# Performance work log

Hardware: AMD Instinct MI355X
Metric: run time of the kernel (lower is better)

The kernel has to match this reference:

```python
import jax, jax.numpy as jnp
import numpy as np

STRIDE = (2, 2)
PADDING = (1, 1)
OUTPUT_PADDING = (0, 0)


def setup_inputs() -> dict:
    key = jax.random.key(0)
    k1, k2, k3 = jax.random.split(key, 3)
    B, Cin, H, W = 16, 32, 128, 128
    Cout, Kh, Kw = 32, 4, 4
    signal = jax.random.normal(k1, (B, Cin, H, W), dtype=jnp.float32)
    # conv_transpose weight layout: (Cin, Cout/groups, Kh, Kw)
    weight = jax.random.normal(k2, (Cin, Cout, Kh, Kw), dtype=jnp.float32) * 0.05
    bias = jax.random.normal(k3, (Cout,), dtype=jnp.float32)
    return {"signal": signal, "weight": weight, "bias": bias}


def reference(signal, weight, bias):
    """FFT-based 2D transposed convolution (stride 2, padding 1, groups=1, dilation=1).

    Matches torch.nn.functional.conv_transpose2d semantics:
      y[n] = sum_m x[m] * w[n - m*s], cropped by `padding` on each side.
    """
    sh, sw = STRIDE
    ph, pw = PADDING
    oph, opw = OUTPUT_PADDING
    B, Cin, H, W = signal.shape
    _, Cout, Kh, Kw = weight.shape

    # 1) zero-stuff the input by the stride (lhs dilation)
    Hu, Wu = (H - 1) * sh + 1, (W - 1) * sw + 1
    xu = jnp.zeros((B, Cin, Hu, Wu), dtype=signal.dtype)
    xu = xu.at[:, :, ::sh, ::sw].set(signal)

    # 2) full (true) convolution of upsampled signal with the weight via rFFT
    Nh, Nw = Hu + Kh - 1, Wu + Kw - 1  # full-conv output size == FFT size
    Xf = jnp.fft.rfft2(xu, s=(Nh, Nw))          # (B, Cin, Nh, Nw//2+1) complex64
    Wf = jnp.fft.rfft2(weight, s=(Nh, Nw))      # (Cin, Cout, Nh, Nw//2+1) complex64
    Yf = jnp.einsum('bihw,iohw->bohw', Xf, Wf)  # contract over input channels
    y = jnp.fft.irfft2(Yf, s=(Nh, Nw))          # (B, Cout, Nh, Nw) float32

    # 3) crop by padding; output_padding extends the end (zero here)
    out_h = (H - 1) * sh - 2 * ph + Kh + oph
    out_w = (W - 1) * sw - 2 * pw + Kw + opw
    y = y[:, :, ph:ph + out_h, pw:pw + out_w]

    # 4) bias
    return y + bias[None, :, None, None]
```

## Files before the change

kernel.cpp:

```cpp
#include <hip/hip_runtime.h>

#define B_    16
#define CIN   32
#define H_    128
#define W_    128
#define COUT  32
#define OH_   256
#define OW_   256

typedef __attribute__((ext_vector_type(8))) short bf8_t;
typedef __attribute__((ext_vector_type(4))) float f32x4;

__device__ inline unsigned int f2bf(float f) {
    unsigned int u = __float_as_uint(f);
    return (u + 0x7fffu + ((u >> 16) & 1u)) >> 16;
}

__global__ __launch_bounds__(256)
void prep_w(const float* __restrict__ wgt, unsigned short* __restrict__ wt) {
    int e = blockIdx.x * 256 + threadIdx.x;
    int khkw = e >> 10, co = (e >> 5) & 31, ci = e & 31;
    wt[e] = (unsigned short)f2bf(wgt[(ci * COUT + co) * 16 + khkw]);
}

__global__ __launch_bounds__(512, 4)
void convt_fused(const float* __restrict__ x,
                 const unsigned short* __restrict__ wt,
                 const float* __restrict__ bias,
                 float* __restrict__ y) {
    __shared__ unsigned short xs[6 * 66 * 32];

    const int tid  = threadIdx.x;
    const int lane = tid & 63;
    const int wv   = tid >> 6;
    const int n    = blockIdx.z;
    const int t0   = blockIdx.y * 4;
    const int u0   = blockIdx.x * 64;

#pragma unroll
    for (int j = 0; j < 3; ++j) {
        const int c  = wv + j * 8;
        const int hr = c >> 2, gp = c & 3;
        const int ih = t0 - 1 + hr;
        const int iw = u0 - 1 + lane;
        const bool inb = ((unsigned)ih < H_) && ((unsigned)iw < W_);
        const float* xq = x + (((long)(n * CIN + gp * 8) * H_ + ih) * W_ + iw);
        float v[8];
#pragma unroll
        for (int k = 0; k < 8; ++k)
            v[k] = inb ? xq[(long)k * (H_ * W_)] : 0.0f;
        uint4 pk;
        pk.x = f2bf(v[0]) | (f2bf(v[1]) << 16);
        pk.y = f2bf(v[2]) | (f2bf(v[3]) << 16);
        pk.z = f2bf(v[4]) | (f2bf(v[5]) << 16);
        pk.w = f2bf(v[6]) | (f2bf(v[7]) << 16);
        const int slot = gp ^ ((iw >> 1) & 3);
        *(uint4*)(xs + (hr * 66 + lane) * 32 + slot * 8) = pk;
    }
    if (tid < 48) {
        const int c  = tid >> 1;
        const int hr = c >> 2, gp = c & 3;
        const int wc = 64 + (tid & 1);
        const int ih = t0 - 1 + hr;
        const int iw = u0 - 1 + wc;
        const bool inb = ((unsigned)ih < H_) && ((unsigned)iw < W_);
        const float* xq = x + (((long)(n * CIN + gp * 8) * H_ + ih) * W_ + iw);
        float v[8];
#pragma unroll
        for (int k = 0; k < 8; ++k)
            v[k] = inb ? xq[(long)k * (H_ * W_)] : 0.0f;
        uint4 pk;
        pk.x = f2bf(v[0]) | (f2bf(v[1]) << 16);
        pk.y = f2bf(v[2]) | (f2bf(v[3]) << 16);
        pk.z = f2bf(v[4]) | (f2bf(v[5]) << 16);
        pk.w = f2bf(v[6]) | (f2bf(v[7]) << 16);
        const int slot = gp ^ ((iw >> 1) & 3);
        *(uint4*)(xs + (hr * 66 + wc) * 32 + slot * 8) = pk;
    }

    const int ch   = wv & 1;
    const int trow = wv >> 1;
    const int g    = lane >> 4;
    const int li   = lane & 15;

    float bias4[4];
#pragma unroll
    for (int r = 0; r < 4; ++r) bias4[r] = bias[ch * 16 + g * 4 + r];

    __syncthreads();

    const int t = t0 + trow;
    const unsigned short* wp = wt + (ch * 16 + li) * 32 + g * 8;

#pragma unroll
    for (int po = 0; po < 2; ++po) {
        const int kh0 = po ? 0 : 1, dh0 = po ? 2 : 1;
        const int kh1 = po ? 2 : 3, dh1 = po ? 1 : 0;

        bf8_t wfA[4], wfB[4];
#pragma unroll
        for (int kw = 0; kw < 4; ++kw) {
            wfA[kw] = *(const bf8_t*)(wp + (kh0 * 4 + kw) * 1024);
            wfB[kw] = *(const bf8_t*)(wp + (kh1 * 4 + kw) * 1024);
        }

#pragma unroll
        for (int st = 0; st < 4; ++st) {
            const int us = u0 + st * 16;

            bf8_t xfA[3], xfB[3];
#pragma unroll
            for (int dw = 0; dw < 3; ++dw) {
                const int wg   = us + li + dw - 1;
                const int wl   = wg - (u0 - 1);
                const int slot = g ^ ((wg >> 1) & 3);
                xfA[dw] = *(const bf8_t*)(xs + ((trow + dh0) * 66 + wl) * 32 + slot * 8);
                xfB[dw] = *(const bf8_t*)(xs + ((trow + dh1) * 66 + wl) * 32 + slot * 8);
            }

            f32x4 acc[2];
#pragma unroll
            for (int qo = 0; qo < 2; ++qo)
                acc[qo] = (f32x4){bias4[0], bias4[1], bias4[2], bias4[3]};

#pragma unroll
            for (int qo = 0; qo < 2; ++qo) {
                const int dw0 = qo ? 2 : 1, kw0 = qo ? 0 : 1;
                const int dw1 = qo ? 1 : 0, kw1 = qo ? 2 : 3;
                acc[qo] = __builtin_amdgcn_mfma_f32_16x16x32_bf16(
                    wfA[kw0], xfA[dw0], acc[qo], 0, 0, 0);
                acc[qo] = __builtin_amdgcn_mfma_f32_16x16x32_bf16(
                    wfA[kw1], xfA[dw1], acc[qo], 0, 0, 0);
                acc[qo] = __builtin_amdgcn_mfma_f32_16x16x32_bf16(
                    wfB[kw0], xfB[dw0], acc[qo], 0, 0, 0);
                acc[qo] = __builtin_amdgcn_mfma_f32_16x16x32_bf16(
                    wfB[kw1], xfB[dw1], acc[qo], 0, 0, 0);
            }

            const int oh = 2 * t + po;
#pragma unroll
            for (int r = 0; r < 4; ++r) {
                const int co = ch * 16 + g * 4 + r;
                float* yp = y + (((long)(n * COUT + co) * OH_ + oh) * OW_) + 2 * (us + li);
                *(float2*)yp = make_float2(acc[0][r], acc[1][r]);
            }
        }
    }
}

extern "C" void kernel_launch(void* const* d_in, const int* in_sizes, int n_in,
                              void* d_out, int out_size, void* d_ws, size_t ws_size,
                              hipStream_t stream) {
    const float* x = (const float*)d_in[0];
    const float* w = (const float*)d_in[1];
    const float* b = (const float*)d_in[2];
    float* y = (float*)d_out;

    unsigned short* wt = (unsigned short*)d_ws;

    prep_w<<<64, 256, 0, stream>>>(w, wt);
    convt_fused<<<dim3(W_ / 64, H_ / 4, B_), 512, 0, stream>>>(x, wt, b, y);
}
```

Before: 169.2 us.

## Double-buffer input tiles so each block prefetches its second row group during compute

```diff
diff --git a/kernel.cpp b/kernel.cpp
--- a/kernel.cpp
+++ b/kernel.cpp
@@ -23,59 +23,114 @@
     wt[e] = (unsigned short)f2bf(wgt[(ci * COUT + co) * 16 + khkw]);
 }
 
+__device__ __forceinline__ void issue8(const float* __restrict__ x, int n, int tt0,
+                                       int u0, int c, int cell, float v[8]) {
+    const int hr = c >> 2, gp = c & 3;
+    const int ih = tt0 - 1 + hr;
+    const int iw = u0 - 1 + cell;
+    const bool inb = ((unsigned)ih < H_) && ((unsigned)iw < W_);
+    const float* xq = x + (((long)(n * CIN + gp * 8) * H_ + ih) * W_ + iw);
+#pragma unroll
+    for (int k = 0; k < 8; ++k)
+        v[k] = inb ? xq[(long)k * (H_ * W_)] : 0.0f;
+}
+
+__device__ __forceinline__ void pack_write(unsigned short* __restrict__ xsb, int u0,
+                                           int c, int cell, const float v[8]) {
+    const int hr = c >> 2, gp = c & 3;
+    const int iw = u0 - 1 + cell;
+    uint4 pk;
+    pk.x = f2bf(v[0]) | (f2bf(v[1]) << 16);
+    pk.y = f2bf(v[2]) | (f2bf(v[3]) << 16);
+    pk.z = f2bf(v[4]) | (f2bf(v[5]) << 16);
+    pk.w = f2bf(v[6]) | (f2bf(v[7]) << 16);
+    const int slot = gp ^ ((iw >> 1) & 3);
+    *(uint4*)(xsb + (hr * 66 + cell) * 32 + slot * 8) = pk;
+}
+
+__device__ __forceinline__ void compute_po(const unsigned short* __restrict__ xsb,
+                                           const unsigned short* __restrict__ wp,
+                                           const float bias4[4], int n, int tt0,
+                                           int trow, int u0, int ch, int g, int li,
+                                           int po, float* __restrict__ y) {
+    const int kh0 = po ? 0 : 1, dh0 = po ? 2 : 1;
+    const int kh1 = po ? 2 : 3, dh1 = po ? 1 : 0;
+
+    bf8_t wfA[4], wfB[4];
+#pragma unroll
+    for (int kw = 0; kw < 4; ++kw) {
+        wfA[kw] = *(const bf8_t*)(wp + (kh0 * 4 + kw) * 1024);
+        wfB[kw] = *(const bf8_t*)(wp + (kh1 * 4 + kw) * 1024);
+    }
+
+    const int t = tt0 + trow;
+#pragma unroll
+    for (int st = 0; st < 4; ++st) {
+        const int us = u0 + st * 16;
+
+        bf8_t xfA[3], xfB[3];
+#pragma unroll
+        for (int dw = 0; dw < 3; ++dw) {
+            const int wg   = us + li + dw - 1;
+            const int wl   = wg - (u0 - 1);
+            const int slot = g ^ ((wg >> 1) & 3);
+            xfA[dw] = *(const bf8_t*)(xsb + ((trow + dh0) * 66 + wl) * 32 + slot * 8);
+            xfB[dw] = *(const bf8_t*)(xsb + ((trow + dh1) * 66 + wl) * 32 + slot * 8);
+        }
+
+        f32x4 acc[2];
+#pragma unroll
+        for (int qo = 0; qo < 2; ++qo)
+            acc[qo] = (f32x4){bias4[0], bias4[1], bias4[2], bias4[3]};
+
+#pragma unroll
+        for (int qo = 0; qo < 2; ++qo) {
+            const int dw0 = qo ? 2 : 1, kw0 = qo ? 0 : 1;
+            const int dw1 = qo ? 1 : 0, kw1 = qo ? 2 : 3;
+            acc[qo] = __builtin_amdgcn_mfma_f32_16x16x32_bf16(
+                wfA[kw0], xfA[dw0], acc[qo], 0, 0, 0);
+            acc[qo] = __builtin_amdgcn_mfma_f32_16x16x32_bf16(
+                wfA[kw1], xfA[dw1], acc[qo], 0, 0, 0);
+            acc[qo] = __builtin_amdgcn_mfma_f32_16x16x32_bf16(
+                wfB[kw0], xfB[dw0], acc[qo], 0, 0, 0);
+            acc[qo] = __builtin_amdgcn_mfma_f32_16x16x32_bf16(
+                wfB[kw1], xfB[dw1], acc[qo], 0, 0, 0);
+        }
+
+        const int oh = 2 * t + po;
+#pragma unroll
+        for (int r = 0; r < 4; ++r) {
+            const int co = ch * 16 + g * 4 + r;
+            float* yp = y + (((long)(n * COUT + co) * OH_ + oh) * OW_) + 2 * (us + li);
+            *(float2*)yp = make_float2(acc[0][r], acc[1][r]);
+        }
+    }
+}
+
 __global__ __launch_bounds__(512, 4)
 void convt_fused(const float* __restrict__ x,
                  const unsigned short* __restrict__ wt,
                  const float* __restrict__ bias,
                  float* __restrict__ y) {
-    __shared__ unsigned short xs[6 * 66 * 32];
+    __shared__ unsigned short xs[2][6 * 66 * 32];
 
     const int tid  = threadIdx.x;
     const int lane = tid & 63;
     const int wv   = tid >> 6;
     const int n    = blockIdx.z;
-    const int t0   = blockIdx.y * 4;
+    const int tb   = blockIdx.y * 8;
     const int u0   = blockIdx.x * 64;
 
 #pragma unroll
     for (int j = 0; j < 3; ++j) {
-        const int c  = wv + j * 8;
-        const int hr = c >> 2, gp = c & 3;
-        const int ih = t0 - 1 + hr;
-        const int iw = u0 - 1 + lane;
-        const bool inb = ((unsigned)ih < H_) && ((unsigned)iw < W_);
-        const float* xq = x + (((long)(n * CIN + gp * 8) * H_ + ih) * W_ + iw);
         float v[8];
-#pragma unroll
-        for (int k = 0; k < 8; ++k)
-            v[k] = inb ? xq[(long)k * (H_ * W_)] : 0.0f;
-        uint4 pk;
-        pk.x = f2bf(v[0]) | (f2bf(v[1]) << 16);
-        pk.y = f2bf(v[2]) | (f2bf(v[3]) << 16);
-        pk.z = f2bf(v[4]) | (f2bf(v[5]) << 16);
-        pk.w = f2bf(v[6]) | (f2bf(v[7]) << 16);
-        const int slot = gp ^ ((iw >> 1) & 3);
-        *(uint4*)(xs + (hr * 66 + lane) * 32 + slot * 8) = pk;
+        issue8(x, n, tb, u0, wv + j * 8, lane, v);
+        pack_write(xs[0], u0, wv + j * 8, lane, v);
     }
     if (tid < 48) {
-        const int c  = tid >> 1;
-        const int hr = c >> 2, gp = c & 3;
-        const int wc = 64 + (tid & 1);
-        const int ih = t0 - 1 + hr;
-        const int iw = u0 - 1 + wc;
-        const bool inb = ((unsigned)ih < H_) && ((unsigned)iw < W_);
-        const float* xq = x + (((long)(n * CIN + gp * 8) * H_ + ih) * W_ + iw);
         float v[8];
-#pragma unroll
-        for (int k = 0; k < 8; ++k)
-            v[k] = inb ? xq[(long)k * (H_ * W_)] : 0.0f;
-        uint4 pk;
-        pk.x = f2bf(v[0]) | (f2bf(v[1]) << 16);
-        pk.y = f2bf(v[2]) | (f2bf(v[3]) << 16);
-        pk.z = f2bf(v[4]) | (f2bf(v[5]) << 16);
-        pk.w = f2bf(v[6]) | (f2bf(v[7]) << 16);
-        const int slot = gp ^ ((iw >> 1) & 3);
-        *(uint4*)(xs + (hr * 66 + wc) * 32 + slot * 8) = pk;
+        issue8(x, n, tb, u0, tid >> 1, 64 + (tid & 1), v);
+        pack_write(xs[0], u0, tid >> 1, 64 + (tid & 1), v);
     }
 
     const int ch   = wv & 1;
@@ -86,66 +141,32 @@
     float bias4[4];
 #pragma unroll
     for (int r = 0; r < 4; ++r) bias4[r] = bias[ch * 16 + g * 4 + r];
+    const unsigned short* wp = wt + (ch * 16 + li) * 32 + g * 8;
 
     __syncthreads();
 
-    const int t = t0 + trow;
-    const unsigned short* wp = wt + (ch * 16 + li) * 32 + g * 8;
+    float vA0[8], vA1[8];
+    issue8(x, n, tb + 4, u0, wv,     lane, vA0);
+    issue8(x, n, tb + 4, u0, wv + 8, lane, vA1);
 
-#pragma unroll
-    for (int po = 0; po < 2; ++po) {
-        const int kh0 = po ? 0 : 1, dh0 = po ? 2 : 1;
-        const int kh1 = po ? 2 : 3, dh1 = po ? 1 : 0;
+    compute_po(xs[0], wp, bias4, n, tb, trow, u0, ch, g, li, 0, y);
 
-        bf8_t wfA[4], wfB[4];
-#pragma unroll
-        for (int kw = 0; kw < 4; ++kw) {
-            wfA[kw] = *(const bf8_t*)(wp + (kh0 * 4 + kw) * 1024);
-            wfB[kw] = *(const bf8_t*)(wp + (kh1 * 4 + kw) * 1024);
-        }
+    pack_write(xs[1], u0, wv,     lane, vA0);
+    pack_write(xs[1], u0, wv + 8, lane, vA1);
+    float vB0[8], vT[8];
+    issue8(x, n, tb + 4, u0, wv + 16, lane, vB0);
+    const bool hasT = (tid < 48);
+    if (hasT) issue8(x, n, tb + 4, u0, tid >> 1, 64 + (tid & 1), vT);
 
-#pragma unroll
-        for (int st = 0; st < 4; ++st) {
-            const int us = u0 + st * 16;
+    compute_po(xs[0], wp, bias4, n, tb, trow, u0, ch, g, li, 1, y);
 
-            bf8_t xfA[3], xfB[3];
-#pragma unroll
-            for (int dw = 0; dw < 3; ++dw) {
-                const int wg   = us + li + dw - 1;
-                const int wl   = wg - (u0 - 1);
-                const int slot = g ^ ((wg >> 1) & 3);
-                xfA[dw] = *(const bf8_t*)(xs + ((trow + dh0) * 66 + wl) * 32 + slot * 8);
-                xfB[dw] = *(const bf8_t*)(xs + ((trow + dh1) * 66 + wl) * 32 + slot * 8);
-            }
+    pack_write(xs[1], u0, wv + 16, lane, vB0);
+    if (hasT) pack_write(xs[1], u0, tid >> 1, 64 + (tid & 1), vT);
 
-            f32x4 acc[2];
-#pragma unroll
-            for (int qo = 0; qo < 2; ++qo)
-                acc[qo] = (f32x4){bias4[0], bias4[1], bias4[2], bias4[3]};
+    __syncthreads();
 
-#pragma unroll
-            for (int qo = 0; qo < 2; ++qo) {
-                const int dw0 = qo ? 2 : 1, kw0 = qo ? 0 : 1;
-                const int dw1 = qo ? 1 : 0, kw1 = qo ? 2 : 3;
-                acc[qo] = __builtin_amdgcn_mfma_f32_16x16x32_bf16(
-                    wfA[kw0], xfA[dw0], acc[qo], 0, 0, 0);
-                acc[qo] = __builtin_amdgcn_mfma_f32_16x16x32_bf16(
-                    wfA[kw1], xfA[dw1], acc[qo], 0, 0, 0);
-                acc[qo] = __builtin_amdgcn_mfma_f32_16x16x32_bf16(
-                    wfB[kw0], xfB[dw0], acc[qo], 0, 0, 0);
-                acc[qo] = __builtin_amdgcn_mfma_f32_16x16x32_bf16(
-                    wfB[kw1], xfB[dw1], acc[qo], 0, 0, 0);
-            }
-
-            const int oh = 2 * t + po;
-#pragma unroll
-            for (int r = 0; r < 4; ++r) {
-                const int co = ch * 16 + g * 4 + r;
-                float* yp = y + (((long)(n * COUT + co) * OH_ + oh) * OW_) + 2 * (us + li);
-                *(float2*)yp = make_float2(acc[0][r], acc[1][r]);
-            }
-        }
-    }
+    compute_po(xs[1], wp, bias4, n, tb + 4, trow, u0, ch, g, li, 0, y);
+    compute_po(xs[1], wp, bias4, n, tb + 4, trow, u0, ch, g, li, 1, y);
 }
 
 extern "C" void kernel_launch(void* const* d_in, const int* in_sizes, int n_in,
@@ -159,5 +180,5 @@
     unsigned short* wt = (unsigned short*)d_ws;
 
     prep_w<<<64, 256, 0, stream>>>(w, wt);
-    convt_fused<<<dim3(W_ / 64, H_ / 4, B_), 512, 0, stream>>>(x, wt, b, y);
+    convt_fused<<<dim3(2, 16, B_), 512, 0, stream>>>(x, wt, b, y);
 }
```

Result: slower. 189.6 us (+12.0%).
